# Kernel tuning notes

Hardware: AMD Instinct MI355X
Metric: run time of the kernel (lower is better)

Reference implementation:

```python
import jax, jax.numpy as jnp
import numpy as np

SEQLEN = 64   # decoder loop length (forward scalar arg)
B = 32        # batch
S = 8192      # context_size (number of context vectors)
D = 256       # hidden_size == context_dim


def setup_inputs() -> dict:
    key = jax.random.key(0)
    k1, k2, k3, k4, k5 = jax.random.split(key, 5)
    hidden = jax.random.normal(k1, (1, B, D), dtype=jnp.float32)
    contextvects = jax.random.normal(k2, (B, D, S), dtype=jnp.float32)
    # nn.Linear(hidden_size=D, context_dim=D): W is [out=D, in=D], b is [D]
    W = jax.random.normal(k3, (D, D), dtype=jnp.float32) / np.sqrt(D).astype(np.float32)
    b = jax.random.normal(k4, (D,), dtype=jnp.float32) * 0.01
    # so no row is fully masked in practice
    padding_mask = jax.random.uniform(k5, (B, S, 1)) < 0.1
    return {"seqlen": SEQLEN, "hidden": hidden, "contextvects": contextvects,
            "W": W, "b": b, "padding_mask": padding_mask}


def reference(seqlen, hidden, contextvects, W, b, padding_mask):
    # context_proj = attn(contextvects.permute(0,2,1)) : [B, S, D]
    # (d = hidden_size input axis, e = context_dim output axis)
    context_proj = jnp.einsum('bds,ed->bse', contextvects, W) + b
    # attn_scores = context_proj @ hidden.permute(1,2,0) : [B, S, 1]
    scores = jnp.matmul(context_proj, jnp.transpose(hidden, (1, 2, 0)))
    scores = jnp.where(padding_mask, -jnp.inf, scores)
    attn = jax.nn.softmax(scores, axis=1)                 # [B, S, 1]
    ctx = jnp.matmul(contextvects, attn)[..., 0]          # [B, D]
    # the torch loop writes identical values for every i in range(seqlen)
    context = jnp.broadcast_to(ctx[None], (seqlen, B, D))
    attentions = jnp.broadcast_to(attn[..., 0][None], (seqlen, B, S))
    return context, attentions
```

## Files before the change

### kernel.cpp

```cpp
#include <hip/hip_runtime.h>
#include <math.h>

#define B_ 32
#define S_ 8192
#define D_ 256
#define TS 64
#define TPB 8
#define BPB (S_ / (TS * TPB))
#define CSHIFT 40.0f

typedef float vf4 __attribute__((ext_vector_type(4)));


__global__ __launch_bounds__(512, 4) void k_fused(const float* __restrict__ cv,
                                                  const float* __restrict__ W,
                                                  const float* __restrict__ h,
                                                  const int* __restrict__ mask,
                                                  float* __restrict__ sc,
                                                  float* __restrict__ lpart,
                                                  float* __restrict__ opart) {
  __shared__ float scw[2][8][64];
  __shared__ float opred[8][512];
  __shared__ float whs[D_];
  __shared__ float hh[D_];

  const int b = blockIdx.y;
  const int blk = blockIdx.x;
  const int t = threadIdx.x;
  const int w = t >> 6;
  const int rq = t >> 4;
  const int cq = t & 15;
  const int mycol = t & 63;
  const int s_base = blk * (TS * TPB);
  const float* cvb = cv + (size_t)b * D_ * S_;

  if (t < D_) hh[t] = h[b * D_ + t];
  __syncthreads();
  if (t < D_) {
    float acc = 0.f;
#pragma unroll 8
    for (int e = 0; e < D_; ++e) acc = fmaf(W[e * D_ + t], hh[e], acc);
    whs[t] = acc;
  }
  __syncthreads();

  float wh8[8];
#pragma unroll
  for (int it = 0; it < 8; ++it) wh8[it] = whs[rq + 32 * it];

  int mpack = 0;
#pragma unroll
  for (int tt = 0; tt < TPB; ++tt)
    if (mask[b * S_ + s_base + tt * TS + mycol] != 0) mpack |= 1 << tt;

  float o[8];
#pragma unroll
  for (int it = 0; it < 8; ++it) o[it] = 0.f;
  float lsum = 0.f;

#pragma unroll 1
  for (int tt = 0; tt < TPB; ++tt) {
    const int c0 = s_base + tt * TS;
    const int pb = tt & 1;

    float4 v[8];
#pragma unroll
    for (int it = 0; it < 8; ++it)
      v[it] = *reinterpret_cast<const float4*>(
          cvb + (size_t)(rq + 32 * it) * S_ + c0 + 4 * cq);

    float4 p; p.x = 0.f; p.y = 0.f; p.z = 0.f; p.w = 0.f;
#pragma unroll
    for (int it = 0; it < 8; ++it) {
      p.x = fmaf(v[it].x, wh8[it], p.x);
      p.y = fmaf(v[it].y, wh8[it], p.y);
      p.z = fmaf(v[it].z, wh8[it], p.z);
      p.w = fmaf(v[it].w, wh8[it], p.w);
    }
    p.x += __shfl_xor(p.x, 16, 64); p.y += __shfl_xor(p.y, 16, 64);
    p.z += __shfl_xor(p.z, 16, 64); p.w += __shfl_xor(p.w, 16, 64);
    p.x += __shfl_xor(p.x, 32, 64); p.y += __shfl_xor(p.y, 32, 64);
    p.z += __shfl_xor(p.z, 32, 64); p.w += __shfl_xor(p.w, 32, 64);
    if ((t & 63) < 16)
      *reinterpret_cast<float4*>(&scw[pb][w][4 * cq]) = p;
    __syncthreads();

    float sv = 0.f;
#pragma unroll
    for (int w2 = 0; w2 < 8; ++w2) sv += scw[pb][w2][mycol];
    if ((mpack >> tt) & 1) sv = -INFINITY;

    const float e = __expf(sv - CSHIFT);
    if (t < 64) sc[(size_t)b * S_ + c0 + t] = e;
    lsum += e;

    const float p0 = __shfl(e, 4 * cq + 0, 64);
    const float p1 = __shfl(e, 4 * cq + 1, 64);
    const float p2 = __shfl(e, 4 * cq + 2, 64);
    const float p3 = __shfl(e, 4 * cq + 3, 64);
#pragma unroll
    for (int it = 0; it < 8; ++it)
      o[it] += v[it].x * p0 + v[it].y * p1 + v[it].z * p2 + v[it].w * p3;
  }

#pragma unroll
  for (int it = 0; it < 8; ++it) opred[it][t] = o[it];
  __syncthreads();
  if (t < 256) {
    float od = 0.f;
    const int k0 = 16 * (t & 31);
    const int itq = t >> 5;
#pragma unroll
    for (int q = 0; q < 16; ++q) od += opred[itq][k0 + q];
    opart[((size_t)b * BPB + blk) * D_ + t] = od;
  }

  if (t < 64) {
    float l = lsum;
#pragma unroll
    for (int off = 32; off > 0; off >>= 1) l += __shfl_xor(l, off, 64);
    if (t == 0) lpart[(size_t)b * BPB + blk] = l;
  }
}

__global__ __launch_bounds__(256) void k_out(const float* __restrict__ lpart,
                                             const float* __restrict__ opart,
                                             const float* __restrict__ sc,
                                             float* __restrict__ out,
                                             int seqlen) {
  const int nAttn = seqlen * B_;
  const int id = blockIdx.x;
  const int t = threadIdx.x;
  __shared__ float sI;

  if (id < nAttn) {
    const int i = id >> 5;
    const int b = id & 31;
    if (t < 64) {
      float lv = (t < BPB) ? lpart[(size_t)b * BPB + t] : 0.f;
#pragma unroll
      for (int off = 32; off > 0; off >>= 1) lv += __shfl_xor(lv, off, 64);
      if (t == 0) sI = 1.0f / lv;
    }
    __syncthreads();
    const float invL = sI;
    vf4* dst = reinterpret_cast<vf4*>(
        out + (size_t)seqlen * B_ * D_ + ((size_t)i * B_ + b) * S_);
    const float4* src = reinterpret_cast<const float4*>(sc + (size_t)b * S_);
#pragma unroll
    for (int j = 0; j < S_ / 4 / 256; ++j) {
      const int q = j * 256 + t;
      const float4 v = src[q];
      vf4 r;
      r.x = v.x * invL;
      r.y = v.y * invL;
      r.z = v.z * invL;
      r.w = v.w * invL;
      __builtin_nontemporal_store(r, &dst[q]);
    }
  } else {
    const int j = id - nAttn;
    const int i = j >> 3;
    const int b = (j & 7) * 4 + (t >> 6);
    const int lane = t & 63;
    float lv = (lane < BPB) ? lpart[(size_t)b * BPB + lane] : 0.f;
#pragma unroll
    for (int off = 32; off > 0; off >>= 1) lv += __shfl_xor(lv, off, 64);
    const float invL = 1.0f / lv;

    vf4 acc = (vf4)0.f;
#pragma unroll
    for (int ti = 0; ti < BPB; ++ti) {
      const float4 op = *reinterpret_cast<const float4*>(
          opart + ((size_t)b * BPB + ti) * D_ + 4 * lane);
      acc.x += op.x; acc.y += op.y; acc.z += op.z; acc.w += op.w;
    }
    acc.x *= invL; acc.y *= invL; acc.z *= invL; acc.w *= invL;
    vf4* cdst = reinterpret_cast<vf4*>(out + ((size_t)i * B_ + b) * D_ + 4 * lane);
    __builtin_nontemporal_store(acc, cdst);
  }
}

extern "C" void kernel_launch(void* const* d_in, const int* in_sizes, int n_in,
                              void* d_out, int out_size, void* d_ws, size_t ws_size,
                              hipStream_t stream) {
  const float* hidden = (const float*)d_in[1];
  const float* cv = (const float*)d_in[2];
  const float* W = (const float*)d_in[3];
  const int* mask = (const int*)d_in[5];

  float* ws = (float*)d_ws;
  float* sc = ws + 16384;
  float* lpart = ws + 278528;
  float* opart = ws + 280576;

  const int seqlen = out_size / (B_ * D_ + B_ * S_);

  k_fused<<<dim3(BPB, B_), 512, 0, stream>>>(cv, W, hidden, mask, sc, lpart, opart);
  k_out<<<seqlen * B_ + seqlen * 8, 256, 0, stream>>>(lpart, opart, sc,
                                                      (float*)d_out, seqlen);
}
```

Before: 69.57 us.

## Fuse score, reduction and broadcast output into one cooperative grid-sync kernel

Replaces the two-kernel pipeline with a single cooperative kernel. Each block computes its slice of scores and partial sums, synchronises across the whole grid, then normalises its own exp values held in registers and writes the broadcast attention and context rows directly. This removes the second launch and the workspace round-trip for unnormalised scores. Each block now covers twice as many tiles so the 8x32 grid can be co-resident. The cost is a grid-wide barrier, plus the output writes being spread over fewer blocks with a longer seqlen loop. If the cooperative launch fails, the old two-kernel path runs instead.

```diff
diff --git a/kernel.cpp b/kernel.cpp
--- a/kernel.cpp
+++ b/kernel.cpp
@@ -1,16 +1,166 @@
 #include <hip/hip_runtime.h>
+#include <hip/hip_cooperative_groups.h>
 #include <math.h>
+
+namespace cg = cooperative_groups;
 
 #define B_ 32
 #define S_ 8192
 #define D_ 256
 #define TS 64
-#define TPB 8
-#define BPB (S_ / (TS * TPB))
 #define CSHIFT 40.0f
 
+#define TPBC 16
+#define BPBC (S_ / (TS * TPBC))
+#define TPBF 8
+#define BPBF (S_ / (TS * TPBF))
+
 typedef float vf4 __attribute__((ext_vector_type(4)));
 
+
+__global__ __launch_bounds__(512, 4) void k_all(const float* __restrict__ cv,
+                                                const float* __restrict__ W,
+                                                const float* __restrict__ h,
+                                                const int* __restrict__ mask,
+                                                float* __restrict__ lpart,
+                                                float* __restrict__ opart,
+                                                float* __restrict__ out,
+                                                int seqlen) {
+  __shared__ float scw[2][8][64];
+  __shared__ float opred[8][512];
+  __shared__ float whs[D_];
+  __shared__ float hh[D_];
+
+  const int b = blockIdx.y;
+  const int blk = blockIdx.x;
+  const int t = threadIdx.x;
+  const int w = t >> 6;
+  const int rq = t >> 4;
+  const int cq = t & 15;
+  const int mycol = t & 63;
+  const int s_base = blk * (TS * TPBC);
+  const float* cvb = cv + (size_t)b * D_ * S_;
+
+  if (t < D_) hh[t] = h[b * D_ + t];
+  __syncthreads();
+  if (t < D_) {
+    float acc = 0.f;
+#pragma unroll 8
+    for (int e = 0; e < D_; ++e) acc = fmaf(W[e * D_ + t], hh[e], acc);
+    whs[t] = acc;
+  }
+  __syncthreads();
+
+  float wh8[8];
+#pragma unroll
+  for (int it = 0; it < 8; ++it) wh8[it] = whs[rq + 32 * it];
+
+  int mpack = 0;
+#pragma unroll
+  for (int tt = 0; tt < TPBC; ++tt)
+    if (mask[b * S_ + s_base + tt * TS + mycol] != 0) mpack |= 1 << tt;
+
+  float o[8];
+#pragma unroll
+  for (int it = 0; it < 8; ++it) o[it] = 0.f;
+  float lsum = 0.f;
+  float ekeep0 = 0.f, ekeep1 = 0.f;
+
+#pragma unroll 1
+  for (int tt = 0; tt < TPBC; ++tt) {
+    const int c0 = s_base + tt * TS;
+    const int pb = tt & 1;
+    float4 v[8];
+#pragma unroll
+    for (int it = 0; it < 8; ++it)
+      v[it] = *reinterpret_cast<const float4*>(
+          cvb + (size_t)(rq + 32 * it) * S_ + c0 + 4 * cq);
+    float4 p; p.x = 0.f; p.y = 0.f; p.z = 0.f; p.w = 0.f;
+#pragma unroll
+    for (int it = 0; it < 8; ++it) {
+      p.x = fmaf(v[it].x, wh8[it], p.x);
+      p.y = fmaf(v[it].y, wh8[it], p.y);
+      p.z = fmaf(v[it].z, wh8[it], p.z);
+      p.w = fmaf(v[it].w, wh8[it], p.w);
+    }
+    p.x += __shfl_xor(p.x, 16, 64); p.y += __shfl_xor(p.y, 16, 64);
+    p.z += __shfl_xor(p.z, 16, 64); p.w += __shfl_xor(p.w, 16, 64);
+    p.x += __shfl_xor(p.x, 32, 64); p.y += __shfl_xor(p.y, 32, 64);
+    p.z += __shfl_xor(p.z, 32, 64); p.w += __shfl_xor(p.w, 32, 64);
+    if ((t & 63) < 16)
+      *reinterpret_cast<float4*>(&scw[pb][w][4 * cq]) = p;
+    __syncthreads();
+    float sv = 0.f;
+#pragma unroll
+    for (int w2 = 0; w2 < 8; ++w2) sv += scw[pb][w2][mycol];
+    if ((mpack >> tt) & 1) sv = -INFINITY;
+    const float e = __expf(sv - CSHIFT);
+    if (tt == w) ekeep0 = e;
+    if (tt == 8 + w) ekeep1 = e;
+    lsum += e;
+    const float p0 = __shfl(e, 4 * cq + 0, 64);
+    const float p1 = __shfl(e, 4 * cq + 1, 64);
+    const float p2 = __shfl(e, 4 * cq + 2, 64);
+    const float p3 = __shfl(e, 4 * cq + 3, 64);
+#pragma unroll
+    for (int it = 0; it < 8; ++it)
+      o[it] += v[it].x * p0 + v[it].y * p1 + v[it].z * p2 + v[it].w * p3;
+  }
+
+#pragma unroll
+  for (int it = 0; it < 8; ++it) opred[it][t] = o[it];
+  __syncthreads();
+  if (t < 256) {
+    float od = 0.f;
+    const int k0 = 16 * (t & 31);
+    const int itq = t >> 5;
+#pragma unroll
+    for (int q = 0; q < 16; ++q) od += opred[itq][k0 + q];
+    opart[((size_t)b * BPBC + blk) * D_ + t] = od;
+  }
+  if (t < 64) {
+    float l = lsum;
+#pragma unroll
+    for (int off = 32; off > 0; off >>= 1) l += __shfl_xor(l, off, 64);
+    if (t == 0) lpart[(size_t)b * BPBC + blk] = l;
+  }
+
+  __threadfence();
+  cg::this_grid().sync();
+
+  float lv = 0.f;
+#pragma unroll
+  for (int i2 = 0; i2 < BPBC; ++i2) lv += lpart[(size_t)b * BPBC + i2];
+  const float invL = 1.0f / lv;
+
+  float* epack = &opred[0][0];
+  epack[t] = ekeep0 * invL;
+  epack[512 + t] = ekeep1 * invL;
+  if (blk == 0 && t < 256) {
+    float acc = 0.f;
+#pragma unroll
+    for (int ti = 0; ti < BPBC; ++ti)
+      acc += opart[((size_t)b * BPBC + ti) * D_ + t];
+    epack[1024 + t] = acc * invL;
+  }
+  __syncthreads();
+
+  {
+    const int q = t & 255;
+    const int g = t >> 8;
+    const vf4 ev = *reinterpret_cast<const vf4*>(&epack[4 * q]);
+    float* outAttn = out + (size_t)seqlen * B_ * D_ + (size_t)b * S_ + s_base + 4 * q;
+    for (int i = g; i < seqlen; i += 2)
+      __builtin_nontemporal_store(ev, reinterpret_cast<vf4*>(outAttn + (size_t)i * B_ * S_));
+  }
+  if (blk == 0) {
+    const int q = t & 63;
+    const int g = t >> 6;
+    const vf4 cv4 = *reinterpret_cast<const vf4*>(&epack[1024 + 4 * q]);
+    for (int i = g; i < seqlen; i += 8)
+      __builtin_nontemporal_store(cv4, reinterpret_cast<vf4*>(out + ((size_t)i * B_ + b) * D_ + 4 * q));
+  }
+}
 
 __global__ __launch_bounds__(512, 4) void k_fused(const float* __restrict__ cv,
                                                   const float* __restrict__ W,
@@ -31,7 +181,7 @@
   const int rq = t >> 4;
   const int cq = t & 15;
   const int mycol = t & 63;
-  const int s_base = blk * (TS * TPB);
+  const int s_base = blk * (TS * TPBF);
   const float* cvb = cv + (size_t)b * D_ * S_;
 
   if (t < D_) hh[t] = h[b * D_ + t];
@@ -50,7 +200,7 @@
 
   int mpack = 0;
 #pragma unroll
-  for (int tt = 0; tt < TPB; ++tt)
+  for (int tt = 0; tt < TPBF; ++tt)
     if (mask[b * S_ + s_base + tt * TS + mycol] != 0) mpack |= 1 << tt;
 
   float o[8];
@@ -59,16 +209,14 @@
   float lsum = 0.f;
 
 #pragma unroll 1
-  for (int tt = 0; tt < TPB; ++tt) {
+  for (int tt = 0; tt < TPBF; ++tt) {
     const int c0 = s_base + tt * TS;
     const int pb = tt & 1;
-
     float4 v[8];
 #pragma unroll
     for (int it = 0; it < 8; ++it)
       v[it] = *reinterpret_cast<const float4*>(
           cvb + (size_t)(rq + 32 * it) * S_ + c0 + 4 * cq);
-
     float4 p; p.x = 0.f; p.y = 0.f; p.z = 0.f; p.w = 0.f;
 #pragma unroll
     for (int it = 0; it < 8; ++it) {
@@ -84,16 +232,13 @@
     if ((t & 63) < 16)
       *reinterpret_cast<float4*>(&scw[pb][w][4 * cq]) = p;
     __syncthreads();
-
     float sv = 0.f;
 #pragma unroll
     for (int w2 = 0; w2 < 8; ++w2) sv += scw[pb][w2][mycol];
     if ((mpack >> tt) & 1) sv = -INFINITY;
-
     const float e = __expf(sv - CSHIFT);
     if (t < 64) sc[(size_t)b * S_ + c0 + t] = e;
     lsum += e;
-
     const float p0 = __shfl(e, 4 * cq + 0, 64);
     const float p1 = __shfl(e, 4 * cq + 1, 64);
     const float p2 = __shfl(e, 4 * cq + 2, 64);
@@ -112,14 +257,13 @@
     const int itq = t >> 5;
 #pragma unroll
     for (int q = 0; q < 16; ++q) od += opred[itq][k0 + q];
-    opart[((size_t)b * BPB + blk) * D_ + t] = od;
-  }
-
+    opart[((size_t)b * BPBF + blk) * D_ + t] = od;
+  }
   if (t < 64) {
     float l = lsum;
 #pragma unroll
     for (int off = 32; off > 0; off >>= 1) l += __shfl_xor(l, off, 64);
-    if (t == 0) lpart[(size_t)b * BPB + blk] = l;
+    if (t == 0) lpart[(size_t)b * BPBF + blk] = l;
   }
 }
 
@@ -137,7 +281,7 @@
     const int i = id >> 5;
     const int b = id & 31;
     if (t < 64) {
-      float lv = (t < BPB) ? lpart[(size_t)b * BPB + t] : 0.f;
+      float lv = (t < BPBF) ? lpart[(size_t)b * BPBF + t] : 0.f;
 #pragma unroll
       for (int off = 32; off > 0; off >>= 1) lv += __shfl_xor(lv, off, 64);
       if (t == 0) sI = 1.0f / lv;
@@ -152,10 +296,7 @@
       const int q = j * 256 + t;
       const float4 v = src[q];
       vf4 r;
-      r.x = v.x * invL;
-      r.y = v.y * invL;
-      r.z = v.z * invL;
-      r.w = v.w * invL;
+      r.x = v.x * invL; r.y = v.y * invL; r.z = v.z * invL; r.w = v.w * invL;
       __builtin_nontemporal_store(r, &dst[q]);
     }
   } else {
@@ -163,16 +304,16 @@
     const int i = j >> 3;
     const int b = (j & 7) * 4 + (t >> 6);
     const int lane = t & 63;
-    float lv = (lane < BPB) ? lpart[(size_t)b * BPB + lane] : 0.f;
+    float lv = (lane < BPBF) ? lpart[(size_t)b * BPBF + lane] : 0.f;
 #pragma unroll
     for (int off = 32; off > 0; off >>= 1) lv += __shfl_xor(lv, off, 64);
     const float invL = 1.0f / lv;
 
     vf4 acc = (vf4)0.f;
 #pragma unroll
-    for (int ti = 0; ti < BPB; ++ti) {
+    for (int ti = 0; ti < BPBF; ++ti) {
       const float4 op = *reinterpret_cast<const float4*>(
-          opart + ((size_t)b * BPB + ti) * D_ + 4 * lane);
+          opart + ((size_t)b * BPBF + ti) * D_ + 4 * lane);
       acc.x += op.x; acc.y += op.y; acc.z += op.z; acc.w += op.w;
     }
     acc.x *= invL; acc.y *= invL; acc.z *= invL; acc.w *= invL;
@@ -193,10 +334,16 @@
   float* sc = ws + 16384;
   float* lpart = ws + 278528;
   float* opart = ws + 280576;
-
-  const int seqlen = out_size / (B_ * D_ + B_ * S_);
-
-  k_fused<<<dim3(BPB, B_), 512, 0, stream>>>(cv, W, hidden, mask, sc, lpart, opart);
-  k_out<<<seqlen * B_ + seqlen * 8, 256, 0, stream>>>(lpart, opart, sc,
-                                                      (float*)d_out, seqlen);
+  float* outp = (float*)d_out;
+  int seqlen = out_size / (B_ * D_ + B_ * S_);
+
+  void* args[] = {(void*)&cv, (void*)&W, (void*)&hidden, (void*)&mask,
+                  (void*)&lpart, (void*)&opart, (void*)&outp, (void*)&seqlen};
+  hipError_t err = hipLaunchCooperativeKernel((const void*)k_all,
+                                              dim3(BPBC, B_), dim3(512),
+                                              args, 0, stream);
+  if (err != hipSuccess) {
+    k_fused<<<dim3(BPBF, B_), 512, 0, stream>>>(cv, W, hidden, mask, sc, lpart, opart);
+    k_out<<<seqlen * B_ + seqlen * 8, 256, 0, stream>>>(lpart, opart, sc, outp, seqlen);
+  }
 }
```

New measurement: 144.1 us. +107.1%, slower.
